# Kernel tuning notes

Hardware: AMD Instinct MI355X
Metric: run time of the kernel (lower is better)

Reference implementation:

```python
import jax, jax.numpy as jnp
import numpy as np

D_MODEL = 1024
N_HEADS = 16
HEAD_SIZE = D_MODEL // N_HEADS
D_FF = 4096
EPS = 1e-6


def _layernorm(x, g, b):
    # Faithful to source: (x + mean) / (std + eps), unbiased std (torch default)
    mean = jnp.mean(x, axis=-1, keepdims=True)
    std = jnp.std(x, axis=-1, keepdims=True, ddof=1)
    return g * ((x + mean) / (std + EPS)) + b


def setup_inputs() -> dict:
    key = jax.random.key(0)
    ks = jax.random.split(key, 12)
    s = lambda fan_in: 1.0 / np.sqrt(fan_in)
    x = jax.random.normal(ks[0], (4, 2048, D_MODEL), dtype=jnp.float32)
    Wq = jax.random.uniform(ks[1], (N_HEADS, D_MODEL, HEAD_SIZE), jnp.float32, -s(D_MODEL), s(D_MODEL))
    Wk = jax.random.uniform(ks[2], (N_HEADS, D_MODEL, HEAD_SIZE), jnp.float32, -s(D_MODEL), s(D_MODEL))
    Wv = jax.random.uniform(ks[3], (N_HEADS, D_MODEL, HEAD_SIZE), jnp.float32, -s(D_MODEL), s(D_MODEL))
    Wo = jax.random.uniform(ks[4], (D_MODEL, D_MODEL), jnp.float32, -s(D_MODEL), s(D_MODEL))
    bo = jax.random.uniform(ks[5], (D_MODEL,), jnp.float32, -s(D_MODEL), s(D_MODEL))
    W1 = jax.random.uniform(ks[6], (D_MODEL, D_FF), jnp.float32, -s(D_MODEL), s(D_MODEL))
    b1 = jax.random.uniform(ks[7], (D_FF,), jnp.float32, -s(D_MODEL), s(D_MODEL))
    W2 = jax.random.uniform(ks[8], (D_FF, D_MODEL), jnp.float32, -s(D_FF), s(D_FF))
    b2 = jax.random.uniform(ks[9], (D_MODEL,), jnp.float32, -s(D_FF), s(D_FF))
    g1 = jnp.ones((D_MODEL,), jnp.float32)
    be1 = jnp.zeros((D_MODEL,), jnp.float32)
    g2 = jnp.ones((D_MODEL,), jnp.float32)
    be2 = jnp.zeros((D_MODEL,), jnp.float32)
    return {"x": x, "Wq": Wq, "Wk": Wk, "Wv": Wv, "Wo": Wo, "bo": bo,
            "W1": W1, "b1": b1, "W2": W2, "b2": b2,
            "g1": g1, "be1": be1, "g2": g2, "be2": be2}


def reference(x, Wq, Wk, Wv, Wo, bo, W1, b1, W2, b2, g1, be1, g2, be2):
    # Multi-head attention; note: source scales by sqrt(d_model), not sqrt(head_size)
    scale = 1.0 / np.sqrt(D_MODEL)
    q = jnp.einsum('bsd,hde->bhse', x, Wq)
    k = jnp.einsum('bsd,hde->bhse', x, Wk)
    v = jnp.einsum('bsd,hde->bhse', x, Wv)
    scores = jnp.einsum('bhse,bhte->bhst', q, k) * scale
    attn = jax.nn.softmax(scores, axis=-1)
    o = jnp.einsum('bhst,bhte->bhse', attn, v)
    B, H, S, E = o.shape
    o = o.transpose(0, 2, 1, 3).reshape(B, S, H * E)  # concat heads
    mha_out = o @ Wo + bo

    h1 = _layernorm(x + mha_out, g1, be1)

    ff = jax.nn.relu(h1 @ W1 + b1) @ W2 + b2
    out = _layernorm(h1 + ff, g2, be2)
    return out
```

## Files before the change

### kernel.cpp

```cpp
#include <hip/hip_runtime.h>

typedef short short8 __attribute__((ext_vector_type(8)));
typedef short short4v __attribute__((ext_vector_type(4)));
typedef float floatx4 __attribute__((ext_vector_type(4)));

#define D_MODEL 1024
#define N_HEADS 16
#define HEAD    64
#define D_FF    4096
#define SEQ     2048
#define BATCH   4
#define TOKENS  (BATCH*SEQ)

__device__ __forceinline__ float b2f(unsigned short u) {
  return __uint_as_float(((unsigned)u) << 16);
}
__device__ __forceinline__ unsigned short f2b(float f) {
  unsigned u = __float_as_uint(f);
  unsigned r = 0x7fffu + ((u >> 16) & 1u);
  return (unsigned short)((u + r) >> 16);
}
__device__ __forceinline__ floatx4 mfma16(short8 a, short8 b, floatx4 c) {
  return __builtin_amdgcn_mfma_f32_16x16x32_bf16(a, b, c, 0, 0, 0);
}
__device__ __forceinline__ void load16_lds(const unsigned short* g, unsigned short* l) {
  __builtin_amdgcn_global_load_lds((const __attribute__((address_space(1))) void*)g,
                                   (__attribute__((address_space(3))) void*)l, 16, 0, 0);
}

__device__ __forceinline__ void transp_body(
    const float* __restrict__ src, unsigned short* __restrict__ dst,
    int R, int C, int bx, int by, float (*t)[65])
{
  int cb = bx * 64, rb = by * 64;
#pragma unroll
  for (int i = 0; i < 16; i++) {
    int idx = i * 256 + threadIdx.x;
    int lr = idx >> 6, lc = idx & 63;
    t[lr][lc] = src[(size_t)(rb + lr) * C + cb + lc];
  }
  __syncthreads();
#pragma unroll
  for (int i = 0; i < 16; i++) {
    int idx = i * 256 + threadIdx.x;
    int lc = idx >> 6, lr = idx & 63;
    dst[(size_t)(cb + lc) * R + rb + lr] = f2b(t[lr][lc]);
  }
}

__global__ __launch_bounds__(256) void prep_kernel(
    const float* __restrict__ x, unsigned short* __restrict__ x_bf,
    const float* __restrict__ Wq, const float* __restrict__ Wk,
    const float* __restrict__ Wv, unsigned short* __restrict__ qkv_bt,
    const float* __restrict__ Wo, unsigned short* __restrict__ wo_bt,
    const float* __restrict__ W1, unsigned short* __restrict__ w1_bt,
    const float* __restrict__ W2, unsigned short* __restrict__ w2_bt)
{
  __shared__ float t[64][65];
  int bid = blockIdx.x;
  if (bid < 8192) {
    int idx = bid * 1024 + threadIdx.x * 4;
    float4 v = *(const float4*)(x + idx);
    short4v o;
    o[0] = (short)f2b(v.x); o[1] = (short)f2b(v.y);
    o[2] = (short)f2b(v.z); o[3] = (short)f2b(v.w);
    *(short4v*)(x_bf + idx) = o;
  } else if (bid < 8960) {
    int by = bid - 8192;
    int xt = by & 15, z = by >> 4;
    int sel = z >> 4, h = z & 15;
    const float* W = (sel == 0) ? Wq : ((sel == 1) ? Wk : Wv);
    const float* src = W + (size_t)h * D_MODEL * HEAD;
    int rb = xt * 64;
#pragma unroll
    for (int i = 0; i < 16; i++) {
      int idx = i * 256 + threadIdx.x;
      int lr = idx >> 6, lc = idx & 63;
      t[lr][lc] = src[(size_t)(rb + lr) * HEAD + lc];
    }
    __syncthreads();
    unsigned short* d0 = qkv_bt + (size_t)(sel * 1024 + h * 64) * D_MODEL;
#pragma unroll
    for (int i = 0; i < 16; i++) {
      int idx = i * 256 + threadIdx.x;
      int lc = idx >> 6, lr = idx & 63;
      d0[(size_t)lc * D_MODEL + rb + lr] = f2b(t[lr][lc]);
    }
  } else if (bid < 9216) {
    int i = bid - 8960;
    transp_body(Wo, wo_bt, 1024, 1024, i & 15, i >> 4, t);
  } else if (bid < 10240) {
    int i = bid - 9216;
    transp_body(W1, w1_bt, 1024, 4096, i & 63, i >> 6, t);
  } else {
    int i = bid - 10240;
    transp_body(W2, w2_bt, 4096, 1024, i & 15, i >> 4, t);
  }
}

__global__ __launch_bounds__(256, 2) void gemm128(
    const unsigned short* __restrict__ A, const unsigned short* __restrict__ BT,
    const float* __restrict__ biasf, const float* __restrict__ residf,
    const unsigned short* __restrict__ residb, void* __restrict__ outp,
    int M, int N, int K, int epi)
{
  __shared__ unsigned short a_sh[2 * 128 * 32];
  __shared__ unsigned short b_sh[2 * 128 * 32];

  const int tid  = threadIdx.x;
  const int lane = tid & 63;
  const int wave = tid >> 6;
  const int quad = lane >> 4;
  const int l15  = lane & 15;
  const int wm   = wave & 1;
  const int wn   = wave >> 1;

  const int lin = blockIdx.y * gridDim.x + blockIdx.x;
  const int xcd = lin & 7, j = lin >> 3;
  const int m0 = (xcd * 8 + (j & 7)) * 128;
  const int n0 = (j >> 3) * 128;

  const int rA = tid >> 2;
  const int kc = (tid & 3) * 8;
  const unsigned short* ag0 = A  + (size_t)(m0 + rA) * K + kc;
  const unsigned short* ag1 = A  + (size_t)(m0 + rA + 64) * K + kc;
  const unsigned short* bg0 = BT + (size_t)(n0 + rA) * K + kc;
  const unsigned short* bg1 = BT + (size_t)(n0 + rA + 64) * K + kc;
  unsigned short* la0 = a_sh + wave * 512;
  unsigned short* la1 = a_sh + 2048 + wave * 512;
  unsigned short* lb0 = b_sh + wave * 512;
  unsigned short* lb1 = b_sh + 2048 + wave * 512;

  floatx4 acc[4][4] = {};

  for (int k0 = 0; k0 < K; k0 += 64) {
    __syncthreads();
    load16_lds(ag0 + k0, la0);
    load16_lds(ag1 + k0, la1);
    load16_lds(bg0 + k0, lb0);
    load16_lds(bg1 + k0, lb1);
    load16_lds(ag0 + k0 + 32, la0 + 4096);
    load16_lds(ag1 + k0 + 32, la1 + 4096);
    load16_lds(bg0 + k0 + 32, lb0 + 4096);
    load16_lds(bg1 + k0 + 32, lb1 + 4096);
    __syncthreads();
#pragma unroll
    for (int h = 0; h < 2; h++) {
      short8 aF[4], bF[4];
#pragma unroll
      for (int i = 0; i < 4; i++)
        aF[i] = *(const short8*)(a_sh + h * 4096 + (wm * 64 + i * 16 + l15) * 32 + quad * 8);
#pragma unroll
      for (int i = 0; i < 4; i++)
        bF[i] = *(const short8*)(b_sh + h * 4096 + (wn * 64 + i * 16 + l15) * 32 + quad * 8);
#pragma unroll
      for (int mi = 0; mi < 4; mi++)
#pragma unroll
        for (int ni = 0; ni < 4; ni++)
          acc[mi][ni] = mfma16(aF[mi], bF[ni], acc[mi][ni]);
    }
  }

#pragma unroll
  for (int mi = 0; mi < 4; mi++) {
#pragma unroll
    for (int ni = 0; ni < 4; ni++) {
      const int col = n0 + wn * 64 + ni * 16 + l15;
      const int row0 = m0 + wm * 64 + mi * 16 + quad * 4;
      if (epi == 0) {
        int sel = col >> 10;
        int cc = col & 1023;
        int h = cc >> 6, e = cc & 63;
        int b = row0 >> 11, s0 = row0 & 2047;
        if (sel < 2) {
          unsigned short* base = (unsigned short*)outp + (size_t)sel * 8388608;
#pragma unroll
          for (int r = 0; r < 4; r++) {
            float v2 = (sel == 0) ? acc[mi][ni][r] * 0.03125f : acc[mi][ni][r];
            base[((size_t)((b * N_HEADS + h) * SEQ + (s0 + r))) * HEAD + e] = f2b(v2);
          }
        } else {
          unsigned short* base = (unsigned short*)outp + (size_t)2 * 8388608;
          short4v pk;
#pragma unroll
          for (int r = 0; r < 4; r++) pk[r] = (short)f2b(acc[mi][ni][r]);
          *(short4v*)(base + ((size_t)((b * N_HEADS + h) * HEAD + e)) * SEQ + s0) = pk;
        }
      } else if (epi == 1) {
#pragma unroll
        for (int r = 0; r < 4; r++)
          ((float*)outp)[(size_t)(row0 + r) * N + col] =
              acc[mi][ni][r] + biasf[col] + residf[(size_t)(row0 + r) * N + col];
      } else if (epi == 2) {
#pragma unroll
        for (int r = 0; r < 4; r++)
          ((unsigned short*)outp)[(size_t)(row0 + r) * N + col] =
              f2b(fmaxf(acc[mi][ni][r] + biasf[col], 0.0f));
      } else {
#pragma unroll
        for (int r = 0; r < 4; r++)
          ((float*)outp)[(size_t)(row0 + r) * N + col] =
              acc[mi][ni][r] + biasf[col] + b2f(residb[(size_t)(row0 + r) * N + col]);
      }
    }
  }
}

__global__ __launch_bounds__(512, 2) void gemm256(
    const unsigned short* __restrict__ A, const unsigned short* __restrict__ BT,
    const float* __restrict__ biasf, void* __restrict__ outp,
    int M, int N, int K, int epi)
{
  __shared__ unsigned short a_sh[2 * 256 * 64];
  __shared__ unsigned short b_sh[2 * 256 * 64];

  const int tid  = threadIdx.x;
  const int lane = tid & 63;
  const int wave = tid >> 6;
  const int quad = lane >> 4;
  const int l15  = lane & 15;
  const int wm   = wave >> 2;
  const int wn   = wave & 3;

  const int lin = blockIdx.y * gridDim.x + blockIdx.x;
  const int xcd = lin & 7, j = lin >> 3;
  const int m0 = (xcd * 4 + (j & 3)) * 256;
  const int n0 = (j >> 2) * 256;

  const int u  = tid >> 3;
  const int sc = (tid & 7) ^ (u & 7);
  const unsigned short* a_src = A  + (size_t)(m0 + u) * K + sc * 8;
  const int borig = ((u >> 5) * 64) + (u & 31);
  const unsigned short* b_src = BT + (size_t)(n0 + borig) * K + sc * 8;
  unsigned short* a_dst = a_sh + wave * 512;
  unsigned short* b_dst = b_sh + wave * 512;

#define SA(T, Rc)  load16_lds(a_src + (size_t)(Rc) * K + (T) * 64, \
                              a_dst + ((T) & 1) * 16384 + (Rc) * 64)
#define SB(T, Rb, Radd) load16_lds(b_src + (size_t)(Radd) * K + (T) * 64, \
                              b_dst + ((T) & 1) * 16384 + (Rb) * 64)
#define STG_A0(T) do { SA(T, 0);   SA(T, 128); } while (0)
#define STG_A1(T) do { SA(T, 64);  SA(T, 192); } while (0)
#define STG_B0(T) do { SB(T, 0, 0);    SB(T, 64, 128); } while (0)
#define STG_B1(T) do { SB(T, 128, 32); SB(T, 192, 160); } while (0)

  floatx4 acc[8][4] = {};
  short8 aF[4][2];
  short8 bF[2][2][2];
  const unsigned short* ash = a_sh;
  const unsigned short* bsh = b_sh;

#define LDA(QM) \
  _Pragma("unroll") for (int mi = 0; mi < 4; mi++) \
  _Pragma("unroll") for (int kh = 0; kh < 2; kh++) \
    aF[mi][kh] = *(const short8*)(ash + (wm * 128 + (QM) * 64 + mi * 16 + l15) * 64 \
                                  + (((kh * 4 + quad) ^ (l15 & 7)) * 8));
#define LDB(QN) \
  _Pragma("unroll") for (int ni = 0; ni < 2; ni++) \
  _Pragma("unroll") for (int kh = 0; kh < 2; kh++) \
    bF[QN][ni][kh] = *(const short8*)(bsh + ((QN) * 128 + wn * 32 + ni * 16 + l15) * 64 \
                                      + (((kh * 4 + quad) ^ (l15 & 7)) * 8));
#define MM(QM, QN) \
  _Pragma("unroll") for (int mi = 0; mi < 4; mi++) \
  _Pragma("unroll") for (int ni = 0; ni < 2; ni++) { \
    acc[(QM) * 4 + mi][(QN) * 2 + ni] = \
        mfma16(aF[mi][0], bF[QN][ni][0], acc[(QM) * 4 + mi][(QN) * 2 + ni]); \
    acc[(QM) * 4 + mi][(QN) * 2 + ni] = \
        mfma16(aF[mi][1], bF[QN][ni][1], acc[(QM) * 4 + mi][(QN) * 2 + ni]); \
  }
#define PH_MID(VMW) \
  asm volatile("s_waitcnt vmcnt(" #VMW ")" ::: "memory"); \
  __builtin_amdgcn_s_barrier(); \
  asm volatile("s_waitcnt lgkmcnt(0)" ::: "memory"); \
  __builtin_amdgcn_sched_barrier(0); \
  __builtin_amdgcn_s_setprio(1);
#define PH_END() \
  __builtin_amdgcn_s_setprio(0); \
  __builtin_amdgcn_s_barrier();

  const int NT = K >> 6;

  STG_A0(0); STG_B0(0); STG_A1(0); STG_B1(0); STG_A0(1); STG_B0(1);
  asm volatile("s_waitcnt vmcnt(8)" ::: "memory");
  __builtin_amdgcn_s_barrier();

  for (int t = 0; t < NT - 2; ++t) {
    ash = a_sh + (t & 1) * 16384;
    bsh = b_sh + (t & 1) * 16384;

    LDA(0) LDB(0)
    STG_A1(t + 1);
    PH_MID(6) MM(0, 0) PH_END();

    LDB(1)
    STG_B1(t + 1);
    PH_MID(6) MM(0, 1) PH_END();

    LDA(1)
    STG_A0(t + 2);
    PH_MID(6) MM(1, 0) PH_END();

    STG_B0(t + 2);
    PH_MID(6) MM(1, 1) PH_END();
  }
  {
    const int t = NT - 2;
    ash = a_sh + (t & 1) * 16384;
    bsh = b_sh + (t & 1) * 16384;

    LDA(0) LDB(0)
    STG_A1(t + 1);
    PH_MID(6) MM(0, 0) PH_END();

    LDB(1)
    STG_B1(t + 1);
    PH_MID(6) MM(0, 1) PH_END();

    LDA(1)
    PH_MID(6) MM(1, 0) PH_END();

    PH_MID(4) MM(1, 1) PH_END();
  }
  {
    const int t = NT - 1;
    ash = a_sh + (t & 1) * 16384;
    bsh = b_sh + (t & 1) * 16384;

    LDA(0) LDB(0)
    PH_MID(0) MM(0, 0) PH_END();

    LDB(1)
    PH_MID(0) MM(0, 1) PH_END();

    LDA(1)
    PH_MID(0) MM(1, 0) PH_END();

    PH_MID(0) MM(1, 1) PH_END();
  }

#undef SA
#undef SB
#undef STG_A0
#undef STG_A1
#undef STG_B0
#undef STG_B1
#undef LDA
#undef LDB
#undef MM
#undef PH_MID
#undef PH_END

#pragma unroll
  for (int mi = 0; mi < 8; mi++) {
#pragma unroll
    for (int ni = 0; ni < 4; ni++) {
      const int col = n0 + wn * 64 + ni * 16 + l15;
      const int row0 = m0 + wm * 128 + mi * 16 + quad * 4;
      if (epi == 0) {
        int sel = col >> 10;
        int cc = col & 1023;
        int h = cc >> 6, e = cc & 63;
        int b = row0 >> 11, s0 = row0 & 2047;
        if (sel < 2) {
          unsigned short* base = (unsigned short*)outp + (size_t)sel * 8388608;
#pragma unroll
          for (int r = 0; r < 4; r++) {
            float v2 = (sel == 0) ? acc[mi][ni][r] * 0.03125f : acc[mi][ni][r];
            base[((size_t)((b * N_HEADS + h) * SEQ + (s0 + r))) * HEAD + e] = f2b(v2);
          }
        } else {
          unsigned short* base = (unsigned short*)outp + (size_t)2 * 8388608;
          short4v pk;
#pragma unroll
          for (int r = 0; r < 4; r++) pk[r] = (short)f2b(acc[mi][ni][r]);
          *(short4v*)(base + ((size_t)((b * N_HEADS + h) * HEAD + e)) * SEQ + s0) = pk;
        }
      } else {
#pragma unroll
        for (int r = 0; r < 4; r++)
          ((unsigned short*)outp)[(size_t)(row0 + r) * N + col] =
              f2b(fmaxf(acc[mi][ni][r] + biasf[col], 0.0f));
      }
    }
  }
}

__global__ __launch_bounds__(256) void attn_kernel(
    const unsigned short* __restrict__ q, const unsigned short* __restrict__ k,
    const unsigned short* __restrict__ vt, unsigned short* __restrict__ o)
{
  const int bh = blockIdx.y;
  const int qt = blockIdx.x;
  const int tid = threadIdx.x, lane = tid & 63, wave = tid >> 6;
  const int quad = lane >> 4, l15 = lane & 15;
  const size_t base = (size_t)bh * SEQ * HEAD;

  __shared__ unsigned short k_sh[64 * 64];
  __shared__ unsigned short vT_sh[64 * 64];
  __shared__ unsigned short p_sh[4 * 32 * 72];
  unsigned short* pw = p_sh + wave * 32 * 72;

  short8 qf[2][2];
#pragma unroll
  for (int mj = 0; mj < 2; mj++) {
    const unsigned short* qp =
        q + base + (size_t)(qt * 128 + wave * 32 + mj * 16 + l15) * HEAD;
    qf[mj][0] = *(const short8*)(qp + quad * 8);
    qf[mj][1] = *(const short8*)(qp + 32 + quad * 8);
  }

  floatx4 oacc[2][4] = {};
  float rs[2] = {0.0f, 0.0f};

  const int r8 = lane >> 3, slot = lane & 7;

  for (int kt = 0; kt < SEQ / 64; kt++) {
    __syncthreads();
#pragma unroll
    for (int i = 0; i < 2; i++) {
      int t = wave * 16 + i * 8 + r8;
      int cg = slot ^ (t & 7);
      load16_lds(k + base + (size_t)(kt * 64 + t) * HEAD + cg * 8,
                 k_sh + (wave * 16 + i * 8) * 64);
      load16_lds(vt + base + (size_t)t * SEQ + kt * 64 + cg * 8,
                 vT_sh + (wave * 16 + i * 8) * 64);
    }
    __syncthreads();

#pragma unroll
    for (int ti = 0; ti < 4; ti++) {
      int t = ti * 16 + l15;
      short8 kf0 = *(const short8*)(k_sh + t * 64 + ((quad ^ (t & 7)) * 8));
      short8 kf1 = *(const short8*)(k_sh + t * 64 + (((4 + quad) ^ (t & 7)) * 8));
      floatx4 s0 = {0.f, 0.f, 0.f, 0.f}, s1 = {0.f, 0.f, 0.f, 0.f};
      s0 = mfma16(kf0, qf[0][0], s0);
      s0 = mfma16(kf1, qf[0][1], s0);
      s1 = mfma16(kf0, qf[1][0], s1);
      s1 = mfma16(kf1, qf[1][1], s1);
#pragma unroll
      for (int mj = 0; mj < 2; mj++) {
        floatx4 s = mj ? s1 : s0;
        float p0 = __expf(s[0]), p1 = __expf(s[1]);
        float p2 = __expf(s[2]), p3 = __expf(s[3]);
        rs[mj] += (p0 + p1) + (p2 + p3);
        uint2 u;
        u.x = __builtin_amdgcn_perm(__float_as_uint(p1), __float_as_uint(p0), 0x07060302u);
        u.y = __builtin_amdgcn_perm(__float_as_uint(p3), __float_as_uint(p2), 0x07060302u);
        *(uint2*)(pw + (mj * 16 + l15) * 72 + ti * 16 + quad * 4) = u;
      }
    }

#pragma unroll
    for (int mj = 0; mj < 2; mj++) {
      short8 pf0 = *(const short8*)(pw + (mj * 16 + l15) * 72 + quad * 8);
      short8 pf1 = *(const short8*)(pw + (mj * 16 + l15) * 72 + 32 + quad * 8);
#pragma unroll
      for (int ni = 0; ni < 4; ni++) {
        int e = ni * 16 + l15;
        short8 bv0 = *(const short8*)(vT_sh + e * 64 + ((quad ^ (e & 7)) * 8));
        short8 bv1 = *(const short8*)(vT_sh + e * 64 + (((4 + quad) ^ (e & 7)) * 8));
        oacc[mj][ni] = mfma16(pf0, bv0, oacc[mj][ni]);
        oacc[mj][ni] = mfma16(pf1, bv1, oacc[mj][ni]);
      }
    }
  }

#pragma unroll
  for (int mj = 0; mj < 2; mj++) {
    rs[mj] += __shfl_xor(rs[mj], 16, 64);
    rs[mj] += __shfl_xor(rs[mj], 32, 64);
  }

  const int b = bh >> 4, h = bh & 15;
#pragma unroll
  for (int mj = 0; mj < 2; mj++)
#pragma unroll
    for (int r = 0; r < 4; r++) {
      int s = qt * 128 + wave * 32 + mj * 16 + quad * 4 + r;
      float inv = 1.0f / __shfl(rs[mj], quad * 4 + r, 64);
#pragma unroll
      for (int ni = 0; ni < 4; ni++)
        o[((size_t)(b * SEQ + s)) * D_MODEL + h * HEAD + ni * 16 + l15] =
            f2b(oacc[mj][ni][r] * inv);
    }
}

__global__ __launch_bounds__(256) void ln_kernel(
    const float* __restrict__ in, const float* __restrict__ g,
    const float* __restrict__ be, void* __restrict__ outp, int write_bf16)
{
  const int row = blockIdx.x * 4 + (threadIdx.x >> 6);
  const int lane = threadIdx.x & 63;
  const float* xp = in + (size_t)row * D_MODEL;
  float4 xv[4];
  float s = 0.0f, ss = 0.0f;
#pragma unroll
  for (int j = 0; j < 4; j++) {
    xv[j] = *(const float4*)(xp + j * 256 + lane * 4);
    s += (xv[j].x + xv[j].y) + (xv[j].z + xv[j].w);
    ss += (xv[j].x * xv[j].x + xv[j].y * xv[j].y) +
          (xv[j].z * xv[j].z + xv[j].w * xv[j].w);
  }
#pragma unroll
  for (int m = 1; m < 64; m <<= 1) {
    s += __shfl_xor(s, m, 64);
    ss += __shfl_xor(ss, m, 64);
  }
  float mean = s * (1.0f / 1024.0f);
  float var = fmaxf((ss - 1024.0f * mean * mean) * (1.0f / 1023.0f), 0.0f);
  float inv = 1.0f / (sqrtf(var) + 1e-6f);
#pragma unroll
  for (int j = 0; j < 4; j++) {
    int c = j * 256 + lane * 4;
    float4 g4 = *(const float4*)(g + c);
    float4 b4 = *(const float4*)(be + c);
    float y0 = g4.x * ((xv[j].x + mean) * inv) + b4.x;
    float y1 = g4.y * ((xv[j].y + mean) * inv) + b4.y;
    float y2 = g4.z * ((xv[j].z + mean) * inv) + b4.z;
    float y3 = g4.w * ((xv[j].w + mean) * inv) + b4.w;
    if (write_bf16) {
      short4v o4;
      o4[0] = (short)f2b(y0); o4[1] = (short)f2b(y1);
      o4[2] = (short)f2b(y2); o4[3] = (short)f2b(y3);
      *(short4v*)((unsigned short*)outp + (size_t)row * D_MODEL + c) = o4;
    } else {
      float4 o4 = {y0, y1, y2, y3};
      *(float4*)((float*)outp + (size_t)row * D_MODEL + c) = o4;
    }
  }
}

extern "C" void kernel_launch(void* const* d_in, const int* in_sizes, int n_in,
                              void* d_out, int out_size, void* d_ws, size_t ws_size,
                              hipStream_t stream)
{
  const float* x   = (const float*)d_in[0];
  const float* Wq  = (const float*)d_in[1];
  const float* Wk  = (const float*)d_in[2];
  const float* Wv  = (const float*)d_in[3];
  const float* Wo  = (const float*)d_in[4];
  const float* bo  = (const float*)d_in[5];
  const float* W1  = (const float*)d_in[6];
  const float* b1  = (const float*)d_in[7];
  const float* W2  = (const float*)d_in[8];
  const float* b2  = (const float*)d_in[9];
  const float* g1  = (const float*)d_in[10];
  const float* be1 = (const float*)d_in[11];
  const float* g2  = (const float*)d_in[12];
  const float* be2 = (const float*)d_in[13];
  float* out = (float*)d_out;

  unsigned short* ws     = (unsigned short*)d_ws;
  unsigned short* w1_bt  = ws;
  unsigned short* w2_bt  = ws + 4194304;
  unsigned short* qkv_bt = ws + 8388608;
  unsigned short* wo_bt  = ws + 11534336;
  unsigned short* x_bf   = ws + 12582912;
  unsigned short* qws    = ws + 20971520;
  unsigned short* kws    = ws + 29360128;
  unsigned short* vws    = ws + 37748736;
  unsigned short* ows    = x_bf;
  float*          r1     = (float*)(ws + 20971520);
  unsigned short* h1_bf  = x_bf;
  unsigned short* ff1    = ws + 20971520;

  dim3 blk(256);

  prep_kernel<<<11264, blk, 0, stream>>>(x, x_bf, Wq, Wk, Wv, qkv_bt,
                                         Wo, wo_bt, W1, w1_bt, W2, w2_bt);

  gemm256<<<dim3(3072 / 256, TOKENS / 256), dim3(512), 0, stream>>>(
      x_bf, qkv_bt, nullptr, qws, TOKENS, 3072, 1024, 0);
  attn_kernel<<<dim3(SEQ / 128, BATCH * N_HEADS), blk, 0, stream>>>(qws, kws, vws, ows);
  gemm128<<<dim3(1024 / 128, TOKENS / 128), blk, 0, stream>>>(
      ows, wo_bt, bo, x, nullptr, r1, TOKENS, 1024, 1024, 1);
  ln_kernel<<<TOKENS / 4, blk, 0, stream>>>(r1, g1, be1, h1_bf, 1);
  gemm256<<<dim3(4096 / 256, TOKENS / 256), dim3(512), 0, stream>>>(
      h1_bf, w1_bt, b1, ff1, TOKENS, 4096, 1024, 2);
  gemm128<<<dim3(1024 / 128, TOKENS / 128), blk, 0, stream>>>(
      ff1, w2_bt, b2, nullptr, h1_bf, out, TOKENS, 1024, 4096, 3);
  ln_kernel<<<TOKENS / 4, blk, 0, stream>>>(out, g2, be2, out, 0);
}
```

Before: 499.3 us.

## Use exp2 with log2e-folded Q scale, MFMA row sums, relaxed GEMM waits

Folds log2(e) into the Q pre-scale so attention can use the hardware exp2 directly instead of __expf. The softmax row sums are now computed with an extra MFMA against a ones vector rather than scalar adds and shuffles. The P·V loop is reordered so each V fragment is reused across both row blocks, and MFMA sections get raised scheduling priority. The big GEMM issues its vmcnt wait only once per k-tile instead of in every phase, and the attention kernel gets an occupancy hint; the looser waits risk LDS races if the counts are wrong.

```diff
diff --git a/kernel.cpp b/kernel.cpp
--- a/kernel.cpp
+++ b/kernel.cpp
@@ -176,7 +176,7 @@
           unsigned short* base = (unsigned short*)outp + (size_t)sel * 8388608;
 #pragma unroll
           for (int r = 0; r < 4; r++) {
-            float v2 = (sel == 0) ? acc[mi][ni][r] * 0.03125f : acc[mi][ni][r];
+            float v2 = (sel == 0) ? acc[mi][ni][r] * 0.04508422f : acc[mi][ni][r];
             base[((size_t)((b * N_HEADS + h) * SEQ + (s0 + r))) * HEAD + e] = f2b(v2);
           }
         } else {
@@ -268,8 +268,8 @@
     acc[(QM) * 4 + mi][(QN) * 2 + ni] = \
         mfma16(aF[mi][1], bF[QN][ni][1], acc[(QM) * 4 + mi][(QN) * 2 + ni]); \
   }
-#define PH_MID(VMW) \
-  asm volatile("s_waitcnt vmcnt(" #VMW ")" ::: "memory"); \
+#define PH_VM(N) asm volatile("s_waitcnt vmcnt(" #N ")" ::: "memory");
+#define PH_MID() \
   __builtin_amdgcn_s_barrier(); \
   asm volatile("s_waitcnt lgkmcnt(0)" ::: "memory"); \
   __builtin_amdgcn_sched_barrier(0); \
@@ -281,7 +281,7 @@
   const int NT = K >> 6;
 
   STG_A0(0); STG_B0(0); STG_A1(0); STG_B1(0); STG_A0(1); STG_B0(1);
-  asm volatile("s_waitcnt vmcnt(8)" ::: "memory");
+  PH_VM(4)
   __builtin_amdgcn_s_barrier();
 
   for (int t = 0; t < NT - 2; ++t) {
@@ -290,18 +290,19 @@
 
     LDA(0) LDB(0)
     STG_A1(t + 1);
-    PH_MID(6) MM(0, 0) PH_END();
+    PH_MID() MM(0, 0) PH_END();
 
     LDB(1)
     STG_B1(t + 1);
-    PH_MID(6) MM(0, 1) PH_END();
+    PH_MID() MM(0, 1) PH_END();
 
     LDA(1)
     STG_A0(t + 2);
-    PH_MID(6) MM(1, 0) PH_END();
+    PH_MID() MM(1, 0) PH_END();
 
     STG_B0(t + 2);
-    PH_MID(6) MM(1, 1) PH_END();
+    PH_VM(4)
+    PH_MID() MM(1, 1) PH_END();
   }
   {
     const int t = NT - 2;
@@ -310,16 +311,17 @@
 
     LDA(0) LDB(0)
     STG_A1(t + 1);
-    PH_MID(6) MM(0, 0) PH_END();
+    PH_MID() MM(0, 0) PH_END();
 
     LDB(1)
     STG_B1(t + 1);
-    PH_MID(6) MM(0, 1) PH_END();
+    PH_MID() MM(0, 1) PH_END();
 
     LDA(1)
-    PH_MID(6) MM(1, 0) PH_END();
-
-    PH_MID(4) MM(1, 1) PH_END();
+    PH_MID() MM(1, 0) PH_END();
+
+    PH_VM(0)
+    PH_MID() MM(1, 1) PH_END();
   }
   {
     const int t = NT - 1;
@@ -327,15 +329,15 @@
     bsh = b_sh + (t & 1) * 16384;
 
     LDA(0) LDB(0)
-    PH_MID(0) MM(0, 0) PH_END();
+    PH_MID() MM(0, 0) PH_END();
 
     LDB(1)
-    PH_MID(0) MM(0, 1) PH_END();
+    PH_MID() MM(0, 1) PH_END();
 
     LDA(1)
-    PH_MID(0) MM(1, 0) PH_END();
-
-    PH_MID(0) MM(1, 1) PH_END();
+    PH_MID() MM(1, 0) PH_END();
+
+    PH_MID() MM(1, 1) PH_END();
   }
 
 #undef SA
@@ -347,6 +349,7 @@
 #undef LDA
 #undef LDB
 #undef MM
+#undef PH_VM
 #undef PH_MID
 #undef PH_END
 
@@ -365,7 +368,7 @@
           unsigned short* base = (unsigned short*)outp + (size_t)sel * 8388608;
 #pragma unroll
           for (int r = 0; r < 4; r++) {
-            float v2 = (sel == 0) ? acc[mi][ni][r] * 0.03125f : acc[mi][ni][r];
+            float v2 = (sel == 0) ? acc[mi][ni][r] * 0.04508422f : acc[mi][ni][r];
             base[((size_t)((b * N_HEADS + h) * SEQ + (s0 + r))) * HEAD + e] = f2b(v2);
           }
         } else {
@@ -385,7 +388,7 @@
   }
 }
 
-__global__ __launch_bounds__(256) void attn_kernel(
+__global__ __launch_bounds__(256, 4) void attn_kernel(
     const unsigned short* __restrict__ q, const unsigned short* __restrict__ k,
     const unsigned short* __restrict__ vt, unsigned short* __restrict__ o)
 {
@@ -410,7 +413,14 @@
   }
 
   floatx4 oacc[2][4] = {};
-  float rs[2] = {0.0f, 0.0f};
+  floatx4 rsacc[2] = {};
+
+  short8 onesf;
+  {
+    short ov = (l15 == 0) ? (short)0x3F80 : (short)0;
+#pragma unroll
+    for (int jj = 0; jj < 8; jj++) onesf[jj] = ov;
+  }
 
   const int r8 = lane >> 3, slot = lane & 7;
 
@@ -433,16 +443,19 @@
       short8 kf0 = *(const short8*)(k_sh + t * 64 + ((quad ^ (t & 7)) * 8));
       short8 kf1 = *(const short8*)(k_sh + t * 64 + (((4 + quad) ^ (t & 7)) * 8));
       floatx4 s0 = {0.f, 0.f, 0.f, 0.f}, s1 = {0.f, 0.f, 0.f, 0.f};
+      __builtin_amdgcn_s_setprio(1);
       s0 = mfma16(kf0, qf[0][0], s0);
       s0 = mfma16(kf1, qf[0][1], s0);
       s1 = mfma16(kf0, qf[1][0], s1);
       s1 = mfma16(kf1, qf[1][1], s1);
+      __builtin_amdgcn_s_setprio(0);
 #pragma unroll
       for (int mj = 0; mj < 2; mj++) {
         floatx4 s = mj ? s1 : s0;
-        float p0 = __expf(s[0]), p1 = __expf(s[1]);
-        float p2 = __expf(s[2]), p3 = __expf(s[3]);
-        rs[mj] += (p0 + p1) + (p2 + p3);
+        float p0 = __builtin_amdgcn_exp2f(s[0]);
+        float p1 = __builtin_amdgcn_exp2f(s[1]);
+        float p2 = __builtin_amdgcn_exp2f(s[2]);
+        float p3 = __builtin_amdgcn_exp2f(s[3]);
         uint2 u;
         u.x = __builtin_amdgcn_perm(__float_as_uint(p1), __float_as_uint(p0), 0x07060302u);
         u.y = __builtin_amdgcn_perm(__float_as_uint(p3), __float_as_uint(p2), 0x07060302u);
@@ -450,25 +463,32 @@
       }
     }
 
-#pragma unroll
-    for (int mj = 0; mj < 2; mj++) {
-      short8 pf0 = *(const short8*)(pw + (mj * 16 + l15) * 72 + quad * 8);
-      short8 pf1 = *(const short8*)(pw + (mj * 16 + l15) * 72 + 32 + quad * 8);
+    {
+      short8 pf[2][2];
+#pragma unroll
+      for (int mj = 0; mj < 2; mj++) {
+        pf[mj][0] = *(const short8*)(pw + (mj * 16 + l15) * 72 + quad * 8);
+        pf[mj][1] = *(const short8*)(pw + (mj * 16 + l15) * 72 + 32 + quad * 8);
+      }
+      __builtin_amdgcn_s_setprio(1);
 #pragma unroll
       for (int ni = 0; ni < 4; ni++) {
         int e = ni * 16 + l15;
         short8 bv0 = *(const short8*)(vT_sh + e * 64 + ((quad ^ (e & 7)) * 8));
         short8 bv1 = *(const short8*)(vT_sh + e * 64 + (((4 + quad) ^ (e & 7)) * 8));
-        oacc[mj][ni] = mfma16(pf0, bv0, oacc[mj][ni]);
-        oacc[mj][ni] = mfma16(pf1, bv1, oacc[mj][ni]);
+#pragma unroll
+        for (int mj = 0; mj < 2; mj++) {
+          oacc[mj][ni] = mfma16(pf[mj][0], bv0, oacc[mj][ni]);
+          oacc[mj][ni] = mfma16(pf[mj][1], bv1, oacc[mj][ni]);
+        }
       }
-    }
-  }
-
-#pragma unroll
-  for (int mj = 0; mj < 2; mj++) {
-    rs[mj] += __shfl_xor(rs[mj], 16, 64);
-    rs[mj] += __shfl_xor(rs[mj], 32, 64);
+#pragma unroll
+      for (int mj = 0; mj < 2; mj++) {
+        rsacc[mj] = mfma16(pf[mj][0], onesf, rsacc[mj]);
+        rsacc[mj] = mfma16(pf[mj][1], onesf, rsacc[mj]);
+      }
+      __builtin_amdgcn_s_setprio(0);
+    }
   }
 
   const int b = bh >> 4, h = bh & 15;
@@ -477,7 +497,8 @@
 #pragma unroll
     for (int r = 0; r < 4; r++) {
       int s = qt * 128 + wave * 32 + mj * 16 + quad * 4 + r;
-      float inv = 1.0f / __shfl(rs[mj], quad * 4 + r, 64);
+      float rsv = __shfl(rsacc[mj][r], quad * 16, 64);
+      float inv = 1.0f / rsv;
 #pragma unroll
       for (int ni = 0; ni < 4; ni++)
         o[((size_t)(b * SEQ + s)) * D_MODEL + h * HEAD + ni * 16 + l15] =
```

Result: no change. 491.9 us (-1.5%).
